# Performance work log

Measured on AMD Instinct MI355X. Metric: run time of the kernel, lower is better.

Reference implementation:

```python
import jax, jax.numpy as jnp
from jax import lax
import numpy as np

H, B, T, E, D, A, C = 4, 32, 1500, 512, 512, 256, 10
KS = 100          # conv_kernel_size
KW = 2 * KS + 1   # filter width = 201
O = 512           # att_odim
SCALING = 2.0


def setup_inputs() -> dict:
    key = jax.random.key(0)
    ks = jax.random.split(key, 12)
    s = 0.05  # param scale to keep tanh in linear-ish regime
    att_prev = jax.random.uniform(ks[3], (H, B, T), dtype=jnp.float32)
    att_prev = att_prev / jnp.sum(att_prev, axis=-1, keepdims=True)  # distribution-like
    return {
        "enc_pad": jax.random.normal(ks[0], (B, T, E), dtype=jnp.float32),
        "enc_len": jnp.full((B,), T, dtype=jnp.int32),
        "dec_z": jax.random.normal(ks[1], (B, D), dtype=jnp.float32),
        "att_prev": att_prev,
        "W_enc": jax.random.normal(ks[4], (H, E, A), dtype=jnp.float32) * s,
        "b_enc": jnp.zeros((H, A), dtype=jnp.float32),
        "W_dec": jax.random.normal(ks[5], (H, D, A), dtype=jnp.float32) * s,
        "W_att": jax.random.normal(ks[6], (H, C, A), dtype=jnp.float32) * s,
        "conv_w": jax.random.normal(ks[7], (H, C, KW), dtype=jnp.float32) * s,
        "gvec_w": jax.random.normal(ks[8], (H, A), dtype=jnp.float32) * s,
        "W_o": jax.random.normal(ks[9], (H * E, O), dtype=jnp.float32) * s,
        "b_o": jnp.zeros((O,), dtype=jnp.float32),
    }


def _loc_conv(att_prev, conv_w):
    # att_prev: [H,B,T], conv_w: [H,C,KW] -> [H,B,C,T]
    def one_head(a, k):  # a [B,T], k [C,KW]
        return lax.conv_general_dilated(
            a[:, None, :], k[:, None, :], (1,), [(KS, KS)],
            dimension_numbers=("NCH", "OIH", "NCH"))  # [B,C,T]
    return jax.vmap(one_head)(att_prev, conv_w)


def reference(enc_pad, enc_len, dec_z, att_prev, W_enc, b_enc, W_dec, W_att,
              conv_w, gvec_w, W_o, b_o):
    # pre-computed encoder projections per head: [H,B,T,A]
    pre_enc = jnp.einsum("bte,hea->hbta", enc_pad, W_enc) + b_enc[:, None, None, :]
    # decoder projection: [H,B,1,A]
    dec_proj = jnp.einsum("bd,hda->hba", dec_z, W_dec)[:, :, None, :]
    # location conv + projection: [H,B,T,A]
    conv_out = _loc_conv(att_prev, conv_w)                       # [H,B,C,T]
    att_conv = jnp.einsum("hbct,hca->hbta", conv_out, W_att)
    # additive scoring: e [H,B,T]
    att_state = jnp.tanh(pre_enc + dec_proj + att_conv)
    e = jnp.einsum("hbta,ha->hbt", att_state, gvec_w)
    w = jax.nn.softmax(SCALING * e, axis=-1)                     # [H,B,T]
    # per-head context: [H,B,E]
    c_heads = jnp.einsum("hbt,bte->hbe", w, enc_pad)
    # concat heads -> [B, H*E], then output projection
    c_cat = jnp.transpose(c_heads, (1, 0, 2)).reshape(B, H * E)
    c = c_cat @ W_o + b_o                                        # [B,O]
    return c, w
```

## Files before the change

### kernel.cpp

```cpp
#include <hip/hip_runtime.h>
#include <hip/hip_bf16.h>

#define NH 4
#define NB 32
#define NT 1500
#define NE 512
#define ND 512
#define NA 256
#define NC 10
#define NKS 100
#define NKW 201
#define NO 512
#define NBT (NB*NT)
#define RB 375
#define OSPLIT 16

#define CV_BLKS 1024
#define DP_BLKS 512
#define PW_BLKS 2176
#define PE_BLKS 6000
#define PREP_BLKS (CV_BLKS + DP_BLKS + PW_BLKS + PE_BLKS)

typedef unsigned short u16;
typedef unsigned int u32;
typedef __attribute__((ext_vector_type(8))) short short8;
typedef __attribute__((ext_vector_type(4))) float f32x4;

__device__ __forceinline__ u16 f2bf(float f) {
  u32 x = __builtin_bit_cast(u32, f);
  return (u16)((x + 0x7FFFu + ((x >> 16) & 1u)) >> 16);
}

__device__ __forceinline__ float bf2f(u16 b) {
  return __builtin_bit_cast(float, (u32)b << 16);
}

__device__ __forceinline__ void gld_lds16(const void* g, void* l) {
  __builtin_amdgcn_global_load_lds((const __attribute__((address_space(1))) u32*)g,
                                   (__attribute__((address_space(3))) u32*)l, 16, 0, 0);
}

__device__ __forceinline__ float fast_tanh(float x) {
  float t, r;
  asm("v_exp_f32 %0, %1" : "=v"(t) : "v"(x * 2.885390082f));
  asm("v_rcp_f32 %0, %1" : "=v"(r) : "v"(t + 1.0f));
  return __builtin_fmaf(-2.0f, r, 1.0f);
}

__global__ __launch_bounds__(256) void k_prep(
    const float* __restrict__ in,
    const float* __restrict__ We, const float* __restrict__ Wa,
    const float* __restrict__ att, const float* __restrict__ cw,
    const float* __restrict__ dz, const float* __restrict__ wd,
    const float* __restrict__ be,
    u16* __restrict__ encb, u16* __restrict__ wc,
    u16* __restrict__ cvb, float* __restrict__ pdp) {
  const int bid = blockIdx.x;
  const int tid = threadIdx.x;
  __shared__ __align__(16) char smem[18944];

  if (bid < CV_BLKS) {
    float* al = (float*)smem;
    float* klT = (float*)(smem + 6016);
    int hb = bid >> 3;
    int h = hb >> 5, b = hb & 31;
    int chunk = bid & 7;
    for (int i = tid; i < NT; i += 256) al[i] = att[(size_t)hb * NT + i];
    for (int i = tid; i < NC * NKW; i += 256)
      klT[(i % NKW) * 16 + (i / NKW)] = cw[h * NC * NKW + i];
    __syncthreads();
    int start = chunk * 188;
    int len = min(188, NT - start);
    if (tid < len) {
      int t = start + tid;
      float acc[NC];
#pragma unroll
      for (int c = 0; c < NC; ++c) acc[c] = 0.f;
      int kmin = max(0, NKS - t);
      int kmax = min(NKW - 1, NT - 1 + NKS - t);
      for (int k = kmin; k <= kmax; ++k) {
        float a = al[t + k - NKS];
        float4 w0 = *(const float4*)&klT[k * 16];
        float4 w1 = *(const float4*)&klT[k * 16 + 4];
        float2 w2 = *(const float2*)&klT[k * 16 + 8];
        acc[0] += a * w0.x; acc[1] += a * w0.y; acc[2] += a * w0.z; acc[3] += a * w0.w;
        acc[4] += a * w1.x; acc[5] += a * w1.y; acc[6] += a * w1.z; acc[7] += a * w1.w;
        acc[8] += a * w2.x; acc[9] += a * w2.y;
      }
      int row = b * NT + t;
      u16* o = cvb + ((size_t)h * NBT + row) * 32;
      short8 g0, g1, gz;
#pragma unroll
      for (int c = 0; c < 8; ++c) g0[c] = (short)f2bf(acc[c]);
      g1[0] = (short)f2bf(acc[8]); g1[1] = (short)f2bf(acc[9]);
#pragma unroll
      for (int c = 2; c < 8; ++c) g1[c] = 0;
#pragma unroll
      for (int c = 0; c < 8; ++c) gz[c] = 0;
      *(short8*)&o[0]  = g0;
      *(short8*)&o[8]  = g1;
      *(short8*)&o[16] = gz;
      *(short8*)&o[24] = gz;
    }
  } else if (bid < CV_BLKS + DP_BLKS) {
    float* z = (float*)smem;
    int id = bid - CV_BLKS;
    int hb = id >> 2, dc = id & 3;
    int h = hb >> 5, b = hb & 31;
    if (tid < 128) z[tid] = dz[b * ND + dc * 128 + tid];
    __syncthreads();
    float s = (dc == 0) ? be[h * NA + tid] : 0.f;
    const float* wp = wd + ((size_t)h * ND + dc * 128) * NA + tid;
    for (int d = 0; d < 128; ++d) s += z[d] * wp[(size_t)d * NA];
    pdp[(((size_t)dc * NH + h) * NB + b) * NA + tid] = s;
  } else if (bid < CV_BLKS + DP_BLKS + PW_BLKS) {
    int idx = (bid - (CV_BLKS + DP_BLKS)) * 256 + tid;
    int h = idx / 139264;
    int r = idx % 139264;
    int kc = r / 2048; r %= 2048;
    int n = r / 8;
    int j = r % 8;
    int k = kc * 8 + j;
    float v = 0.f;
    if (k < NE) v = We[((size_t)h * NE + k) * NA + n];
    else if (k - NE < NC) v = Wa[((size_t)h * NC + (k - NE)) * NA + n];
    wc[idx] = f2bf(v);
  } else {
    int id = bid - (CV_BLKS + DP_BLKS + PW_BLKS);
    size_t i0 = ((size_t)id * 256 + tid) * 16;
    const float4* s = (const float4*)(in + i0);
    float4 v0 = s[0], v1 = s[1], v2 = s[2], v3 = s[3];
    short8 a, b;
    a[0] = (short)f2bf(v0.x); a[1] = (short)f2bf(v0.y);
    a[2] = (short)f2bf(v0.z); a[3] = (short)f2bf(v0.w);
    a[4] = (short)f2bf(v1.x); a[5] = (short)f2bf(v1.y);
    a[6] = (short)f2bf(v1.z); a[7] = (short)f2bf(v1.w);
    b[0] = (short)f2bf(v2.x); b[1] = (short)f2bf(v2.y);
    b[2] = (short)f2bf(v2.z); b[3] = (short)f2bf(v2.w);
    b[4] = (short)f2bf(v3.x); b[5] = (short)f2bf(v3.y);
    b[6] = (short)f2bf(v3.z); b[7] = (short)f2bf(v3.w);
    *(short8*)(encb + i0) = a;
    *(short8*)(encb + i0 + 8) = b;
  }
}

__global__ __launch_bounds__(512) void k_gemm_e(
    const u16* __restrict__ encb, const u16* __restrict__ cvb,
    const u16* __restrict__ wcomb, const float* __restrict__ pdp,
    const float* __restrict__ gvec, float* __restrict__ ebuf) {
  const int orig = blockIdx.x;
  const int xcd = orig & 7, pos = orig >> 3;
  const int wgid = (xcd < 4 ? xcd * 188 : 752 + (xcd - 4) * 187) + pos;
  const int h = wgid & 3;
  const int rowblk = wgid >> 2;
  const int row0 = rowblk * 128;
  const int tid = threadIdx.x;
  const int lane = tid & 63;
  const int wid = tid >> 6;
  const int wm = wid >> 2;
  const int wn = wid & 3;
  const int l16 = lane & 15;
  const int lh = lane >> 4;

  __shared__ u16 Alds[3][4096];
  __shared__ u16 Blds[3][8192];
  __shared__ float dp[2][NA];
  __shared__ float gl[NA];
  __shared__ float elds[128][4];

  const int b0 = row0 / NT;
  const int bound = (b0 + 1) * NT - row0;
  const int b1 = min(b0 + 1, NB - 1);
  if (tid < NA) {
    float s = 0.f;
#pragma unroll
    for (int dc = 0; dc < 4; ++dc)
      s += pdp[(((size_t)dc * NH + h) * NB + b0) * NA + tid];
    dp[0][tid] = s;
    gl[tid] = gvec[h * NA + tid];
  } else {
    int a = tid - NA;
    float s = 0.f;
#pragma unroll
    for (int dc = 0; dc < 4; ++dc)
      s += pdp[(((size_t)dc * NH + h) * NB + b1) * NA + a];
    dp[1][a] = s;
  }

  f32x4 acc[4][4] = {};

  const u16* aBase = encb + (size_t)(row0 + (tid >> 2)) * NE + (tid & 3) * 8;
  const u16* aTail = cvb + ((size_t)h * NBT + row0) * 32 + tid * 8;
  const u16* bSrc = wcomb + (size_t)h * 139264;

  const int arow = wm * 64 + l16;
  const int bcol = wn * 64 + l16;

#define ISSUE(is, buf) do {                                         \
    const u16* ga_ = ((is) < 16) ? (aBase + (is) * 32) : aTail;     \
    gld_lds16(ga_, &Alds[(buf)][tid * 8]);                          \
    const u16* gb_ = bSrc + (is) * 8192;                            \
    gld_lds16(gb_ + tid * 8, &Blds[(buf)][tid * 8]);                \
    gld_lds16(gb_ + 4096 + tid * 8, &Blds[(buf)][4096 + tid * 8]);  \
  } while (0)

  ISSUE(0, 0);
  ISSUE(1, 1);

  int cur = 0;
  for (int ks = 0; ks < 17; ++ks) {
    if (ks < 16) asm volatile("s_waitcnt vmcnt(3)" ::: "memory");
    else         asm volatile("s_waitcnt vmcnt(0)" ::: "memory");
    __builtin_amdgcn_s_barrier();
    __builtin_amdgcn_sched_barrier(0);
    if (ks + 2 <= 16) {
      int nbuf = (cur + 2 >= 3) ? cur - 1 : cur + 2;
      ISSUE(ks + 2, nbuf);
    }
    const u16* ap = &Alds[cur][arow * 32 + lh * 8];
    const u16* bp = &Blds[cur][(lh * 256 + bcol) * 8];
    short8 af[4], bf4[4];
#pragma unroll
    for (int i = 0; i < 4; ++i) af[i] = *(const short8*)&ap[i * 512];
#pragma unroll
    for (int i = 0; i < 4; ++i) bf4[i] = *(const short8*)&bp[i * 128];
    __builtin_amdgcn_s_setprio(1);
#pragma unroll
    for (int i = 0; i < 4; ++i)
#pragma unroll
      for (int j = 0; j < 4; ++j)
        acc[i][j] = __builtin_amdgcn_mfma_f32_16x16x32_bf16(af[i], bf4[j], acc[i][j], 0, 0, 0);
    __builtin_amdgcn_s_setprio(0);
    cur = (cur == 2) ? 0 : cur + 1;
  }
#undef ISSUE
  __syncthreads();

  float ep[4][4];
#pragma unroll
  for (int i = 0; i < 4; ++i)
#pragma unroll
    for (int r = 0; r < 4; ++r) ep[i][r] = 0.f;

#pragma unroll
  for (int j = 0; j < 4; ++j) {
    int col = wn * 64 + j * 16 + l16;
    float g = gl[col];
    float biasLo = dp[0][col], biasHi = dp[1][col];
#pragma unroll
    for (int i = 0; i < 4; ++i) {
#pragma unroll
      for (int r = 0; r < 4; ++r) {
        int rl = wm * 64 + i * 16 + lh * 4 + r;
        float bias = (rl >= bound) ? biasHi : biasLo;
        ep[i][r] += g * fast_tanh(acc[i][j][r] + bias);
      }
    }
  }
#pragma unroll
  for (int d = 1; d < 16; d <<= 1)
#pragma unroll
    for (int i = 0; i < 4; ++i)
#pragma unroll
      for (int r = 0; r < 4; ++r) ep[i][r] += __shfl_xor(ep[i][r], d, 64);

  if (l16 == 0) {
#pragma unroll
    for (int i = 0; i < 4; ++i)
#pragma unroll
      for (int r = 0; r < 4; ++r) elds[wm * 64 + i * 16 + lh * 4 + r][wn] = ep[i][r];
  }
  __syncthreads();
  if (tid < 128) {
    float e = elds[tid][0] + elds[tid][1] + elds[tid][2] + elds[tid][3];
    ebuf[(size_t)h * NBT + row0 + tid] = e;
  }
}

__global__ __launch_bounds__(512) void k_context(const u16* __restrict__ encb,
                                                 const float* __restrict__ ebuf,
                                                 float* __restrict__ wout,
                                                 float* __restrict__ part) {
  int b = blockIdx.x, ch = blockIdx.y;
  int tid = threadIdx.x;
  int g = tid >> 6;
  int lane = tid & 63;
  __shared__ float el[NH][NT];
  __shared__ float wl[NH][192];
  __shared__ float redw[NH][8];

#pragma unroll
  for (int hh = 0; hh < NH; ++hh)
    for (int t = tid; t < NT; t += 512)
      el[hh][t] = ebuf[((size_t)hh * NB + b) * NT + t];
  __syncthreads();

  float mx[NH];
#pragma unroll
  for (int hh = 0; hh < NH; ++hh) {
    float m = -1e30f;
    for (int t = tid; t < NT; t += 512) m = fmaxf(m, el[hh][t]);
#pragma unroll
    for (int d = 1; d < 64; d <<= 1) m = fmaxf(m, __shfl_xor(m, d, 64));
    if (lane == 0) redw[hh][g] = m;
  }
  __syncthreads();
#pragma unroll
  for (int hh = 0; hh < NH; ++hh) {
    float m = redw[hh][0];
#pragma unroll
    for (int i = 1; i < 8; ++i) m = fmaxf(m, redw[hh][i]);
    mx[hh] = m;
  }
  __syncthreads();
  float inv[NH];
#pragma unroll
  for (int hh = 0; hh < NH; ++hh) {
    float s = 0.f;
    for (int t = tid; t < NT; t += 512) s += expf(2.f * (el[hh][t] - mx[hh]));
#pragma unroll
    for (int d = 1; d < 64; d <<= 1) s += __shfl_xor(s, d, 64);
    if (lane == 0) redw[hh][g] = s;
  }
  __syncthreads();
#pragma unroll
  for (int hh = 0; hh < NH; ++hh) {
    float s = redw[hh][0];
#pragma unroll
    for (int i = 1; i < 8; ++i) s += redw[hh][i];
    inv[hh] = 1.f / s;
  }

  int c0 = ch * 188;
  int n = min(188, NT - c0);
#pragma unroll
  for (int hh = 0; hh < NH; ++hh) {
    for (int tt = tid; tt < 188; tt += 512) {
      float w = 0.f;
      if (tt < n) {
        w = expf(2.f * (el[hh][c0 + tt] - mx[hh])) * inv[hh];
        wout[((size_t)hh * NB + b) * NT + c0 + tt] = w;
      }
      wl[hh][tt] = w;
    }
  }
  __syncthreads();

  float acc[NH][8];
#pragma unroll
  for (int hh = 0; hh < NH; ++hh)
#pragma unroll
    for (int j = 0; j < 8; ++j) acc[hh][j] = 0.f;

  for (int tt = g; tt < n; tt += 8) {
    size_t row = (size_t)b * NT + c0 + tt;
    const u16* src = encb + row * NE + lane * 8;
    short8 v = *(const short8*)src;
    float f[8];
#pragma unroll
    for (int j = 0; j < 8; ++j) f[j] = bf2f((u16)v[j]);
#pragma unroll
    for (int hh = 0; hh < NH; ++hh) {
      float ww = wl[hh][tt];
#pragma unroll
      for (int j = 0; j < 8; ++j) acc[hh][j] += ww * f[j];
    }
  }
  __shared__ float red[8][NE];
#pragma unroll
  for (int hh = 0; hh < NH; ++hh) {
    __syncthreads();
#pragma unroll
    for (int j = 0; j < 8; ++j) red[g][lane * 8 + j] = acc[hh][j];
    __syncthreads();
    float s = red[0][tid] + red[1][tid] + red[2][tid] + red[3][tid]
            + red[4][tid] + red[5][tid] + red[6][tid] + red[7][tid];
    part[((size_t)(ch * NH + hh) * NB + b) * NE + tid] = s;
  }
}

__global__ __launch_bounds__(512) void k_out_part(const float* __restrict__ part,
                                                  const float* __restrict__ Wo,
                                                  float* __restrict__ pout) {
  int b = blockIdx.x, is = blockIdx.y;
  int tid = threadIdx.x;
  int i0 = is * 128;
  __shared__ float cc[128];
  if (tid < 128) {
    int i = i0 + tid;
    int hh = i >> 9, ee = i & 511;
    float s = 0.f;
#pragma unroll
    for (int ch = 0; ch < 8; ++ch)
      s += part[((size_t)(ch * NH + hh) * NB + b) * NE + ee];
    cc[tid] = s;
  }
  __syncthreads();
  float acc = 0.f;
  const float* wp = Wo + (size_t)i0 * NO + tid;
#pragma unroll 4
  for (int il = 0; il < 128; il += 4) {
    float4 v = *(const float4*)&cc[il];
    acc += v.x * wp[(size_t)(il + 0) * NO];
    acc += v.y * wp[(size_t)(il + 1) * NO];
    acc += v.z * wp[(size_t)(il + 2) * NO];
    acc += v.w * wp[(size_t)(il + 3) * NO];
  }
  pout[((size_t)is * NB + b) * NO + tid] = acc;
}

__global__ __launch_bounds__(512) void k_out_red(const float* __restrict__ pout,
                                                 const float* __restrict__ bo,
                                                 float* __restrict__ cout) {
  int b = blockIdx.x, tid = threadIdx.x;
  float acc = bo[tid];
#pragma unroll
  for (int is = 0; is < OSPLIT; ++is)
    acc += pout[((size_t)is * NB + b) * NO + tid];
  cout[(size_t)b * NO + tid] = acc;
}

extern "C" void kernel_launch(void* const* d_in, const int* in_sizes, int n_in,
                              void* d_out, int out_size, void* d_ws, size_t ws_size,
                              hipStream_t stream) {
  const float* enc      = (const float*)d_in[0];
  const float* dec_z    = (const float*)d_in[2];
  const float* att_prev = (const float*)d_in[3];
  const float* W_enc    = (const float*)d_in[4];
  const float* b_enc    = (const float*)d_in[5];
  const float* W_dec    = (const float*)d_in[6];
  const float* W_att    = (const float*)d_in[7];
  const float* conv_w   = (const float*)d_in[8];
  const float* gvec_w   = (const float*)d_in[9];
  const float* W_o      = (const float*)d_in[10];
  const float* b_o      = (const float*)d_in[11];
  float* cout = (float*)d_out;
  float* wout = (float*)d_out + NB * NO;

  char* ws = (char*)d_ws;
  size_t off = 0;
  u16* encb   = (u16*)(ws + off); off += (size_t)NBT * NE * 2;
  u16* cvb    = (u16*)(ws + off); off += (size_t)NH * NBT * 32 * 2;
  u16* wcomb  = (u16*)(ws + off); off += (size_t)NH * 139264 * 2;
  float* pdp   = (float*)(ws + off); off += (size_t)4 * NH * NB * NA * 4;
  float* ebuf  = (float*)(ws + off); off += (size_t)NH * NB * NT * 4;
  float* part  = (float*)(ws + off); off += (size_t)8 * NH * NB * NE * 4;
  float* pout  = (float*)(ws + off); off += (size_t)OSPLIT * NB * NO * 4;

  hipLaunchKernelGGL(k_prep, dim3(PREP_BLKS), dim3(256), 0, stream,
                     enc, W_enc, W_att, att_prev, conv_w, dec_z, W_dec, b_enc,
                     encb, wcomb, cvb, pdp);
  hipLaunchKernelGGL(k_gemm_e, dim3(1500), dim3(512), 0, stream,
                     encb, cvb, wcomb, pdp, gvec_w, ebuf);
  hipLaunchKernelGGL(k_context, dim3(32, 8), dim3(512), 0, stream,
                     encb, ebuf, wout, part);
  hipLaunchKernelGGL(k_out_part, dim3(NB, OSPLIT), dim3(512), 0, stream, part, W_o, pout);
  hipLaunchKernelGGL(k_out_red, dim3(NB), dim3(512), 0, stream, pout, b_o, cout);
}
```

Baseline: 132.4 us.

## Fuse fp32-to-bf16 encoder conversion into GEMM A-tile loading with register prefetch

Removes the separate pass that converts the encoder activations to bf16 and writes them to a workspace. The GEMM kernel now loads fp32 rows into registers one stage ahead, converts them, and stores them into an XOR-swizzled LDS tile. Only the B tiles still use direct global-to-LDS loads. The context kernel reads the fp32 encoder directly, and the conv output is stored as fp32. The aim is to cut the extra read and write traffic of the prep pass, at the cost of twice the A-load bytes in the GEMM, extra register pressure, and conversion ALU work inside the main loop.

Result: slower. 186.1 us (+40.6%).

```diff
diff --git a/kernel.cpp b/kernel.cpp
--- a/kernel.cpp
+++ b/kernel.cpp
@@ -12,14 +12,12 @@
 #define NKW 201
 #define NO 512
 #define NBT (NB*NT)
-#define RB 375
 #define OSPLIT 16
 
 #define CV_BLKS 1024
 #define DP_BLKS 512
 #define PW_BLKS 2176
-#define PE_BLKS 6000
-#define PREP_BLKS (CV_BLKS + DP_BLKS + PW_BLKS + PE_BLKS)
+#define PREP_BLKS (CV_BLKS + DP_BLKS + PW_BLKS)
 
 typedef unsigned short u16;
 typedef unsigned int u32;
@@ -29,10 +27,6 @@
 __device__ __forceinline__ u16 f2bf(float f) {
   u32 x = __builtin_bit_cast(u32, f);
   return (u16)((x + 0x7FFFu + ((x >> 16) & 1u)) >> 16);
-}
-
-__device__ __forceinline__ float bf2f(u16 b) {
-  return __builtin_bit_cast(float, (u32)b << 16);
 }
 
 __device__ __forceinline__ void gld_lds16(const void* g, void* l) {
@@ -48,13 +42,11 @@
 }
 
 __global__ __launch_bounds__(256) void k_prep(
-    const float* __restrict__ in,
     const float* __restrict__ We, const float* __restrict__ Wa,
     const float* __restrict__ att, const float* __restrict__ cw,
     const float* __restrict__ dz, const float* __restrict__ wd,
     const float* __restrict__ be,
-    u16* __restrict__ encb, u16* __restrict__ wc,
-    u16* __restrict__ cvb, float* __restrict__ pdp) {
+    u16* __restrict__ wc, float* __restrict__ cvf, float* __restrict__ pdp) {
   const int bid = blockIdx.x;
   const int tid = threadIdx.x;
   __shared__ __align__(16) char smem[18944];
@@ -88,19 +80,15 @@
         acc[8] += a * w2.x; acc[9] += a * w2.y;
       }
       int row = b * NT + t;
-      u16* o = cvb + ((size_t)h * NBT + row) * 32;
-      short8 g0, g1, gz;
-#pragma unroll
-      for (int c = 0; c < 8; ++c) g0[c] = (short)f2bf(acc[c]);
-      g1[0] = (short)f2bf(acc[8]); g1[1] = (short)f2bf(acc[9]);
-#pragma unroll
-      for (int c = 2; c < 8; ++c) g1[c] = 0;
-#pragma unroll
-      for (int c = 0; c < 8; ++c) gz[c] = 0;
-      *(short8*)&o[0]  = g0;
-      *(short8*)&o[8]  = g1;
-      *(short8*)&o[16] = gz;
-      *(short8*)&o[24] = gz;
+      float* o = cvf + ((size_t)h * NBT + row) * 32;
+      float4 w0 = {acc[0], acc[1], acc[2], acc[3]};
+      float4 w1 = {acc[4], acc[5], acc[6], acc[7]};
+      float4 w2 = {acc[8], acc[9], 0.f, 0.f};
+      float4 z4 = {0.f, 0.f, 0.f, 0.f};
+      ((float4*)o)[0] = w0; ((float4*)o)[1] = w1;
+      ((float4*)o)[2] = w2; ((float4*)o)[3] = z4;
+      ((float4*)o)[4] = z4; ((float4*)o)[5] = z4;
+      ((float4*)o)[6] = z4; ((float4*)o)[7] = z4;
     }
   } else if (bid < CV_BLKS + DP_BLKS) {
     float* z = (float*)smem;
@@ -113,7 +101,7 @@
     const float* wp = wd + ((size_t)h * ND + dc * 128) * NA + tid;
     for (int d = 0; d < 128; ++d) s += z[d] * wp[(size_t)d * NA];
     pdp[(((size_t)dc * NH + h) * NB + b) * NA + tid] = s;
-  } else if (bid < CV_BLKS + DP_BLKS + PW_BLKS) {
+  } else {
     int idx = (bid - (CV_BLKS + DP_BLKS)) * 256 + tid;
     int h = idx / 139264;
     int r = idx % 139264;
@@ -125,27 +113,11 @@
     if (k < NE) v = We[((size_t)h * NE + k) * NA + n];
     else if (k - NE < NC) v = Wa[((size_t)h * NC + (k - NE)) * NA + n];
     wc[idx] = f2bf(v);
-  } else {
-    int id = bid - (CV_BLKS + DP_BLKS + PW_BLKS);
-    size_t i0 = ((size_t)id * 256 + tid) * 16;
-    const float4* s = (const float4*)(in + i0);
-    float4 v0 = s[0], v1 = s[1], v2 = s[2], v3 = s[3];
-    short8 a, b;
-    a[0] = (short)f2bf(v0.x); a[1] = (short)f2bf(v0.y);
-    a[2] = (short)f2bf(v0.z); a[3] = (short)f2bf(v0.w);
-    a[4] = (short)f2bf(v1.x); a[5] = (short)f2bf(v1.y);
-    a[6] = (short)f2bf(v1.z); a[7] = (short)f2bf(v1.w);
-    b[0] = (short)f2bf(v2.x); b[1] = (short)f2bf(v2.y);
-    b[2] = (short)f2bf(v2.z); b[3] = (short)f2bf(v2.w);
-    b[4] = (short)f2bf(v3.x); b[5] = (short)f2bf(v3.y);
-    b[6] = (short)f2bf(v3.z); b[7] = (short)f2bf(v3.w);
-    *(short8*)(encb + i0) = a;
-    *(short8*)(encb + i0 + 8) = b;
   }
 }
 
 __global__ __launch_bounds__(512) void k_gemm_e(
-    const u16* __restrict__ encb, const u16* __restrict__ cvb,
+    const float* __restrict__ enc, const float* __restrict__ cvf,
     const u16* __restrict__ wcomb, const float* __restrict__ pdp,
     const float* __restrict__ gvec, float* __restrict__ ebuf) {
   const int orig = blockIdx.x;
@@ -162,8 +134,8 @@
   const int l16 = lane & 15;
   const int lh = lane >> 4;
 
-  __shared__ u16 Alds[3][4096];
-  __shared__ u16 Blds[3][8192];
+  __shared__ u16 AldsF[3 * 4096];
+  __shared__ u16 BldsF[3 * 8192];
   __shared__ float dp[2][NA];
   __shared__ float gl[NA];
   __shared__ float elds[128][4];
@@ -189,51 +161,87 @@
 
   f32x4 acc[4][4] = {};
 
-  const u16* aBase = encb + (size_t)(row0 + (tid >> 2)) * NE + (tid & 3) * 8;
-  const u16* aTail = cvb + ((size_t)h * NBT + row0) * 32 + tid * 8;
+  const int wrow = tid >> 2;
+  const int c8 = tid & 3;
+  const float* aEnc = enc + (size_t)(row0 + wrow) * NE + c8 * 8;
+  const float* aCvf = cvf + ((size_t)h * NBT + row0 + wrow) * 32 + c8 * 8;
+  const int awOff = wrow * 32 + (c8 ^ ((wrow >> 1) & 3)) * 8;
   const u16* bSrc = wcomb + (size_t)h * 139264;
 
   const int arow = wm * 64 + l16;
   const int bcol = wn * 64 + l16;
-
-#define ISSUE(is, buf) do {                                         \
-    const u16* ga_ = ((is) < 16) ? (aBase + (is) * 32) : aTail;     \
-    gld_lds16(ga_, &Alds[(buf)][tid * 8]);                          \
-    const u16* gb_ = bSrc + (is) * 8192;                            \
-    gld_lds16(gb_ + tid * 8, &Blds[(buf)][tid * 8]);                \
-    gld_lds16(gb_ + 4096 + tid * 8, &Blds[(buf)][4096 + tid * 8]);  \
+  const int achunk = lh ^ ((arow >> 1) & 3);
+
+  float4 aPlo, aPhi, aNlo, aNhi;
+
+  {
+    float4 t0lo = ((const float4*)aEnc)[0];
+    float4 t0hi = ((const float4*)aEnc)[1];
+    gld_lds16(bSrc + tid * 8, BldsF + tid * 8);
+    gld_lds16(bSrc + 4096 + tid * 8, BldsF + 4096 + tid * 8);
+    aPlo = ((const float4*)(aEnc + 32))[0];
+    aPhi = ((const float4*)(aEnc + 32))[1];
+    gld_lds16(bSrc + 8192 + tid * 8, BldsF + 8192 + tid * 8);
+    gld_lds16(bSrc + 8192 + 4096 + tid * 8, BldsF + 8192 + 4096 + tid * 8);
+    short8 s;
+    s[0] = (short)f2bf(t0lo.x); s[1] = (short)f2bf(t0lo.y);
+    s[2] = (short)f2bf(t0lo.z); s[3] = (short)f2bf(t0lo.w);
+    s[4] = (short)f2bf(t0hi.x); s[5] = (short)f2bf(t0hi.y);
+    s[6] = (short)f2bf(t0hi.z); s[7] = (short)f2bf(t0hi.w);
+    *(short8*)&AldsF[awOff] = s;
+  }
+
+  int ks = 0, cur = 0;
+
+#define ITER(APlo, APhi, ANlo, ANhi) do {                                    \
+    if (ks < 16) asm volatile("s_waitcnt vmcnt(4) lgkmcnt(0)" ::: "memory"); \
+    else         asm volatile("s_waitcnt vmcnt(0) lgkmcnt(0)" ::: "memory"); \
+    __builtin_amdgcn_s_barrier();                                            \
+    __builtin_amdgcn_sched_barrier(0);                                       \
+    if (ks + 2 <= 16) {                                                      \
+      const float* ga_ = (ks + 2 < 16) ? (aEnc + (ks + 2) * 32) : aCvf;      \
+      ANlo = ((const float4*)ga_)[0];                                        \
+      ANhi = ((const float4*)ga_)[1];                                        \
+      int nbuf_ = cur + 2; if (nbuf_ >= 3) nbuf_ -= 3;                       \
+      const u16* gb_ = bSrc + (ks + 2) * 8192;                               \
+      gld_lds16(gb_ + tid * 8, BldsF + nbuf_ * 8192 + tid * 8);              \
+      gld_lds16(gb_ + 4096 + tid * 8, BldsF + nbuf_ * 8192 + 4096 + tid * 8);\
+    }                                                                        \
+    {                                                                        \
+      const u16* ap_ = AldsF + cur * 4096 + arow * 32 + achunk * 8;          \
+      const u16* bp_ = BldsF + cur * 8192 + (lh * 256 + bcol) * 8;           \
+      short8 af[4], bf4[4];                                                  \
+      _Pragma("unroll")                                                      \
+      for (int i = 0; i < 4; ++i) af[i] = *(const short8*)&ap_[i * 512];     \
+      _Pragma("unroll")                                                      \
+      for (int i = 0; i < 4; ++i) bf4[i] = *(const short8*)&bp_[i * 128];    \
+      __builtin_amdgcn_s_setprio(1);                                         \
+      _Pragma("unroll")                                                      \
+      for (int i = 0; i < 4; ++i)                                            \
+        _Pragma("unroll")                                                    \
+        for (int j = 0; j < 4; ++j)                                          \
+          acc[i][j] = __builtin_amdgcn_mfma_f32_16x16x32_bf16(af[i], bf4[j], \
+                                                              acc[i][j], 0, 0, 0); \
+      __builtin_amdgcn_s_setprio(0);                                         \
+    }                                                                        \
+    if (ks <= 15) {                                                          \
+      int wbuf_ = cur + 1; if (wbuf_ >= 3) wbuf_ -= 3;                       \
+      short8 s_;                                                             \
+      s_[0] = (short)f2bf(APlo.x); s_[1] = (short)f2bf(APlo.y);              \
+      s_[2] = (short)f2bf(APlo.z); s_[3] = (short)f2bf(APlo.w);              \
+      s_[4] = (short)f2bf(APhi.x); s_[5] = (short)f2bf(APhi.y);              \
+      s_[6] = (short)f2bf(APhi.z); s_[7] = (short)f2bf(APhi.w);              \
+      *(short8*)&AldsF[wbuf_ * 4096 + awOff] = s_;                           \
+    }                                                                        \
+    ++ks; cur = (cur == 2) ? 0 : cur + 1;                                    \
   } while (0)
 
-  ISSUE(0, 0);
-  ISSUE(1, 1);
-
-  int cur = 0;
-  for (int ks = 0; ks < 17; ++ks) {
-    if (ks < 16) asm volatile("s_waitcnt vmcnt(3)" ::: "memory");
-    else         asm volatile("s_waitcnt vmcnt(0)" ::: "memory");
-    __builtin_amdgcn_s_barrier();
-    __builtin_amdgcn_sched_barrier(0);
-    if (ks + 2 <= 16) {
-      int nbuf = (cur + 2 >= 3) ? cur - 1 : cur + 2;
-      ISSUE(ks + 2, nbuf);
-    }
-    const u16* ap = &Alds[cur][arow * 32 + lh * 8];
-    const u16* bp = &Blds[cur][(lh * 256 + bcol) * 8];
-    short8 af[4], bf4[4];
-#pragma unroll
-    for (int i = 0; i < 4; ++i) af[i] = *(const short8*)&ap[i * 512];
-#pragma unroll
-    for (int i = 0; i < 4; ++i) bf4[i] = *(const short8*)&bp[i * 128];
-    __builtin_amdgcn_s_setprio(1);
-#pragma unroll
-    for (int i = 0; i < 4; ++i)
-#pragma unroll
-      for (int j = 0; j < 4; ++j)
-        acc[i][j] = __builtin_amdgcn_mfma_f32_16x16x32_bf16(af[i], bf4[j], acc[i][j], 0, 0, 0);
-    __builtin_amdgcn_s_setprio(0);
-    cur = (cur == 2) ? 0 : cur + 1;
-  }
-#undef ISSUE
+  for (int kp = 0; kp < 8; ++kp) {
+    ITER(aPlo, aPhi, aNlo, aNhi);
+    ITER(aNlo, aNhi, aPlo, aPhi);
+  }
+  ITER(aPlo, aPhi, aNlo, aNhi);
+#undef ITER
   __syncthreads();
 
   float ep[4][4];
@@ -277,7 +285,7 @@
   }
 }
 
-__global__ __launch_bounds__(512) void k_context(const u16* __restrict__ encb,
+__global__ __launch_bounds__(512) void k_context(const float* __restrict__ enc,
                                                  const float* __restrict__ ebuf,
                                                  float* __restrict__ wout,
                                                  float* __restrict__ part) {
@@ -354,11 +362,10 @@
 
   for (int tt = g; tt < n; tt += 8) {
     size_t row = (size_t)b * NT + c0 + tt;
-    const u16* src = encb + row * NE + lane * 8;
-    short8 v = *(const short8*)src;
-    float f[8];
-#pragma unroll
-    for (int j = 0; j < 8; ++j) f[j] = bf2f((u16)v[j]);
+    const float* src = enc + row * NE + lane * 8;
+    float4 v0 = ((const float4*)src)[0];
+    float4 v1 = ((const float4*)src)[1];
+    float f[8] = {v0.x, v0.y, v0.z, v0.w, v1.x, v1.y, v1.z, v1.w};
 #pragma unroll
     for (int hh = 0; hh < NH; ++hh) {
       float ww = wl[hh][tt];
@@ -439,21 +446,20 @@
 
   char* ws = (char*)d_ws;
   size_t off = 0;
-  u16* encb   = (u16*)(ws + off); off += (size_t)NBT * NE * 2;
-  u16* cvb    = (u16*)(ws + off); off += (size_t)NH * NBT * 32 * 2;
-  u16* wcomb  = (u16*)(ws + off); off += (size_t)NH * 139264 * 2;
+  float* cvf   = (float*)(ws + off); off += (size_t)NH * NBT * 32 * 4;
+  u16* wcomb   = (u16*)(ws + off);  off += (size_t)NH * 139264 * 2;
   float* pdp   = (float*)(ws + off); off += (size_t)4 * NH * NB * NA * 4;
   float* ebuf  = (float*)(ws + off); off += (size_t)NH * NB * NT * 4;
   float* part  = (float*)(ws + off); off += (size_t)8 * NH * NB * NE * 4;
   float* pout  = (float*)(ws + off); off += (size_t)OSPLIT * NB * NO * 4;
 
   hipLaunchKernelGGL(k_prep, dim3(PREP_BLKS), dim3(256), 0, stream,
-                     enc, W_enc, W_att, att_prev, conv_w, dec_z, W_dec, b_enc,
-                     encb, wcomb, cvb, pdp);
+                     W_enc, W_att, att_prev, conv_w, dec_z, W_dec, b_enc,
+                     wcomb, cvf, pdp);
   hipLaunchKernelGGL(k_gemm_e, dim3(1500), dim3(512), 0, stream,
-                     encb, cvb, wcomb, pdp, gvec_w, ebuf);
+                     enc, cvf, wcomb, pdp, gvec_w, ebuf);
   hipLaunchKernelGGL(k_context, dim3(32, 8), dim3(512), 0, stream,
-                     encb, ebuf, wout, part);
+                     enc, ebuf, wout, part);
   hipLaunchKernelGGL(k_out_part, dim3(NB, OSPLIT), dim3(512), 0, stream, part, W_o, pout);
   hipLaunchKernelGGL(k_out_red, dim3(NB), dim3(512), 0, stream, pout, b_o, cout);
 }
```
